# Kernel tuning notes

Hardware: AMD Instinct MI355X
Metric: run time of the kernel (lower is better)

## Reference

```python
import jax, jax.numpy as jnp
import numpy as np

N = 100000      # nodes
E = 1600000     # edges
F_IN = 128
HID = 64
N_CLS = 40


def setup_inputs() -> dict:
    key = jax.random.key(0)
    ks = jax.random.split(key, 8)
    x = jax.random.normal(ks[0], (N, F_IN), dtype=jnp.float32)
    edge_index = jax.random.randint(ks[1], (2, E), 0, N, dtype=jnp.int64)
    # SAGEConv params: lin_l (applied to mean-aggregated neighbors, with bias),
    # lin_r (applied to root/self features, no bias). Glorot-ish init scaling.
    W1_l = jax.random.normal(ks[2], (F_IN, HID), dtype=jnp.float32) / np.sqrt(F_IN)
    b1 = jnp.zeros((HID,), dtype=jnp.float32)
    W1_r = jax.random.normal(ks[3], (F_IN, HID), dtype=jnp.float32) / np.sqrt(F_IN)
    W2_l = jax.random.normal(ks[4], (HID, N_CLS), dtype=jnp.float32) / np.sqrt(HID)
    b2 = jnp.zeros((N_CLS,), dtype=jnp.float32)
    W2_r = jax.random.normal(ks[5], (HID, N_CLS), dtype=jnp.float32) / np.sqrt(HID)
    return {"x": x, "edge_index": edge_index,
            "W1_l": W1_l, "b1": b1, "W1_r": W1_r,
            "W2_l": W2_l, "b2": b2, "W2_r": W2_r}


def _sage_conv(x, src, dst, W_l, b_l, W_r):
    # mean aggregation of neighbor features: messages flow src -> dst
    msgs = x[src]                                              # [E, d]
    summed = jax.ops.segment_sum(msgs, dst, num_segments=N)    # [N, d]
    cnt = jax.ops.segment_sum(jnp.ones((src.shape[0],), x.dtype), dst,
                              num_segments=N)                  # [N]
    agg = summed / jnp.maximum(cnt, 1.0)[:, None]
    return agg @ W_l + b_l + x @ W_r


def reference(x, edge_index, W1_l, b1, W1_r, W2_l, b2, W2_r):
    src, dst = edge_index[0], edge_index[1]
    h = jax.nn.relu(_sage_conv(x, src, dst, W1_l, b1, W1_r))
    # dropout: identity in eval mode
    logits = _sage_conv(h, src, dst, W2_l, b2, W2_r)
    return jax.nn.log_softmax(logits, axis=1)
```

## Files before the change

### kernel.cpp

```cpp
#include <hip/hip_runtime.h>
#include <math.h>

#define N_NODES 100000
#define F_IN    128
#define HID     64
#define N_CLS   40
#define MT      (N_NODES / 16)

#define BSHIFT  9
#define BSZ     512
#define NB      ((N_NODES + BSZ - 1) / BSZ)
#define EPB     4096

typedef __attribute__((ext_vector_type(8))) short bf8_t;
typedef __attribute__((ext_vector_type(4))) float f4_t;
typedef __attribute__((ext_vector_type(2))) float f2v_t;

typedef unsigned short ushort_t;
typedef unsigned int uint_t;
typedef unsigned char uchar_t;

__device__ __forceinline__ ushort_t f2b(float f) {
    union { float f; uint_t u; } c; c.f = f;
    uint_t u = c.u + 0x7FFFu + ((c.u >> 16) & 1u);
    return (ushort_t)(u >> 16);
}
__device__ __forceinline__ float b2f(ushort_t h) {
    union { uint_t u; float f; } c; c.u = ((uint_t)h) << 16;
    return c.f;
}

#if defined(__has_builtin)
#if __has_builtin(__builtin_amdgcn_cvt_pk_f32_fp8) && __has_builtin(__builtin_amdgcn_cvt_pk_fp8_f32)
#define HAVE_FP8_HW 1
#endif
#endif

__device__ __forceinline__ uchar_t fp8_enc(float v) {
#ifdef HAVE_FP8_HW
    return (uchar_t)(__builtin_amdgcn_cvt_pk_fp8_f32(v, v, 0, false) & 0xff);
#else
    union { float f; uint_t u; } c; c.f = v;
    uint_t s = c.u >> 31;
    float av = fabsf(v);
    if (av > 448.f) av = 448.f;
    int e;
    float m = frexpf(av, &e);
    int ee = e + 6;
    uchar_t r;
    if (av == 0.f) r = 0;
    else if (ee <= 0) {
        int q = (int)(av * 512.f + 0.5f);
        if (q > 7) q = 7;
        r = (uchar_t)q;
    } else {
        int q = (int)(m * 16.f + 0.5f);
        if (q == 16) { q = 8; ee += 1; }
        if (ee > 15) { ee = 15; q = 15; }
        r = (uchar_t)((ee << 3) | (q & 7));
    }
    return r | (uchar_t)(s << 7);
#endif
}

__device__ __forceinline__ f2v_t fp8x2_dec_lo(uint_t w) {
#ifdef HAVE_FP8_HW
    return __builtin_amdgcn_cvt_pk_f32_fp8(w, false);
#else
    f2v_t r;
    for (int k = 0; k < 2; ++k) {
        uchar_t b = (w >> (8 * k)) & 0xff;
        uint_t s = (b >> 7) & 1, e = (b >> 3) & 15, m = b & 7;
        float f;
        if (e) { union { uint_t u; float ff; } c;
                 c.u = (s << 31) | ((e + 120) << 23) | (m << 20); f = c.ff; }
        else   { f = (float)m * 0.001953125f; if (s) f = -f; }
        r[k] = f;
    }
    return r;
#endif
}
__device__ __forceinline__ f2v_t fp8x2_dec_hi(uint_t w) {
#ifdef HAVE_FP8_HW
    return __builtin_amdgcn_cvt_pk_f32_fp8(w, true);
#else
    return fp8x2_dec_lo(w >> 16);
#endif
}

__global__ void block_hist_kernel(const int* __restrict__ ei, int E,
                                  int* __restrict__ blockHist) {
    __shared__ int cnt[NB];
    int t = threadIdx.x, blk = blockIdx.x;
    for (int i = t; i < NB; i += 256) cnt[i] = 0;
    __syncthreads();
    int e0 = blk * EPB;
#pragma unroll
    for (int i = 0; i < EPB / 256; ++i) {
        int e = e0 + i * 256 + t;
        if (e < E) atomicAdd(&cnt[ei[E + e] >> BSHIFT], 1);
    }
    __syncthreads();
    for (int i = t; i < NB; i += 256) blockHist[blk * NB + i] = cnt[i];
}

__global__ void col_scan_kernel(const int* __restrict__ blockHist, int nblk,
                                int* __restrict__ blockBase,
                                int* __restrict__ btot) {
    __shared__ int ss[256];
    __shared__ int carry;
    int bin = blockIdx.x, t = threadIdx.x;
    if (t == 0) carry = 0;
    __syncthreads();
    for (int c0 = 0; c0 < nblk; c0 += 256) {
        int b = c0 + t;
        int v = (b < nblk) ? blockHist[b * NB + bin] : 0;
        ss[t] = v;
        __syncthreads();
        for (int off = 1; off < 256; off <<= 1) {
            int u = (t >= off) ? ss[t - off] : 0;
            __syncthreads();
            ss[t] += u;
            __syncthreads();
        }
        if (b < nblk) blockBase[b * NB + bin] = carry + ss[t] - v;
        __syncthreads();
        if (t == 255) carry += ss[255];
        __syncthreads();
    }
    if (t == 0) btot[bin] = carry;
}

__global__ void bucket_scan_kernel(const int* __restrict__ btot,
                                   int* __restrict__ boff,
                                   int* __restrict__ rowptr) {
    __shared__ int ss[256];
    int t = threadIdx.x;
    int v = (t < NB) ? btot[t] : 0;
    ss[t] = v;
    __syncthreads();
    for (int off = 1; off < 256; off <<= 1) {
        int u = (t >= off) ? ss[t - off] : 0;
        __syncthreads();
        ss[t] += u;
        __syncthreads();
    }
    if (t < NB) boff[t] = ss[t] - v;
    if (t == NB - 1) rowptr[N_NODES] = ss[t];
}

__global__ void scatter_pairs_kernel(const int* __restrict__ ei, int E,
                                     const int* __restrict__ blockBase,
                                     const int* __restrict__ boff,
                                     uint_t* __restrict__ pairs) {
    __shared__ int cur[NB];
    __shared__ int base[NB];
    int t = threadIdx.x, blk = blockIdx.x;
    for (int i = t; i < NB; i += 256) {
        cur[i] = 0;
        base[i] = boff[i] + blockBase[blk * NB + i];
    }
    __syncthreads();
    int e0 = blk * EPB;
#pragma unroll
    for (int i = 0; i < EPB / 256; ++i) {
        int e = e0 + i * 256 + t;
        if (e < E) {
            int src = ei[e];
            int dst = ei[E + e];
            int bin = dst >> BSHIFT;
            int r = atomicAdd(&cur[bin], 1);
            pairs[base[bin] + r] = ((uint_t)src << BSHIFT) | (uint_t)(dst & (BSZ - 1));
        }
    }
}

__global__ void bucket_sort_kernel(const uint_t* __restrict__ pairs,
                                   const int* __restrict__ boff,
                                   const int* __restrict__ btot,
                                   int* __restrict__ rowptr,
                                   int* __restrict__ csr) {
    __shared__ int hist[BSZ];
    __shared__ int lofs[BSZ];
    int bin = blockIdx.x, t = threadIdx.x;
    int base = boff[bin], cnt = btot[bin];
    hist[t] = 0;
    __syncthreads();
    for (int i = t; i < cnt; i += BSZ)
        atomicAdd(&hist[pairs[base + i] & (BSZ - 1)], 1);
    __syncthreads();
    int v = hist[t];
    lofs[t] = v;
    __syncthreads();
    for (int off = 1; off < BSZ; off <<= 1) {
        int u = (t >= off) ? lofs[t - off] : 0;
        __syncthreads();
        lofs[t] += u;
        __syncthreads();
    }
    int excl = lofs[t] - v;
    int d_global = (bin << BSHIFT) + t;
    if (d_global < N_NODES) rowptr[d_global] = base + excl;
    __syncthreads();
    lofs[t] = excl;
    hist[t] = 0;
    __syncthreads();
    for (int i = t; i < cnt; i += BSZ) {
        uint_t p = pairs[base + i];
        int lb = p & (BSZ - 1);
        int r = atomicAdd(&hist[lb], 1);
        csr[base + lofs[lb] + r] = (int)(p >> BSHIFT);
    }
}

__global__ void cvt_w_kernel(const float* __restrict__ W1l,
                             const float* __restrict__ W1r,
                             const float* __restrict__ W2l,
                             const float* __restrict__ W2r,
                             ushort_t* __restrict__ W1t,
                             ushort_t* __restrict__ W2t) {
    int t = blockIdx.x * blockDim.x + threadIdx.x;
    if (t < 128 * F_IN) {
        int n = t / F_IN, k = t - n * F_IN;
        float v = (n < HID) ? W1l[k * HID + n] : W1r[k * HID + (n - HID)];
        W1t[t] = f2b(v);
    } else if (t < 128 * F_IN + 80 * HID) {
        int u = t - 128 * F_IN;
        int n = u / HID, k = u - n * HID;
        float v = (n < N_CLS) ? W2l[k * N_CLS + n] : W2r[k * N_CLS + (n - N_CLS)];
        W2t[u] = f2b(v);
    }
}

__global__ void gemm1_mfma_kernel(const float* __restrict__ x,
                                  const ushort_t* __restrict__ W1t,
                                  uchar_t* __restrict__ y1a,
                                  uchar_t* __restrict__ y1b,
                                  ushort_t* __restrict__ z1b) {
    int gid = blockIdx.x * blockDim.x + threadIdx.x;
    int wave = gid >> 6, lane = gid & 63;
    if (wave >= MT) return;
    int m0 = wave * 16;
    int r = lane & 15, q = lane >> 4;

    const float* xr = x + (size_t)(m0 + r) * F_IN + q * 8;
    bf8_t a[4];
#pragma unroll
    for (int kt = 0; kt < 4; ++kt) {
        float4 u = *(const float4*)(xr + kt * 32);
        float4 v = *(const float4*)(xr + kt * 32 + 4);
        bf8_t t;
        t[0] = (short)f2b(u.x); t[1] = (short)f2b(u.y);
        t[2] = (short)f2b(u.z); t[3] = (short)f2b(u.w);
        t[4] = (short)f2b(v.x); t[5] = (short)f2b(v.y);
        t[6] = (short)f2b(v.z); t[7] = (short)f2b(v.w);
        a[kt] = t;
    }
#pragma unroll
    for (int tn = 0; tn < 8; ++tn) {
        const ushort_t* wr = W1t + (size_t)(tn * 16 + r) * F_IN + q * 8;
        f4_t acc = {0.f, 0.f, 0.f, 0.f};
#pragma unroll
        for (int kt = 0; kt < 4; ++kt) {
            bf8_t b = *(const bf8_t*)(wr + kt * 32);
            acc = __builtin_amdgcn_mfma_f32_16x16x32_bf16(a[kt], b, acc, 0, 0, 0);
        }
        int col = tn * 16 + r;
        if (col < 32) {
#pragma unroll
            for (int rr = 0; rr < 4; ++rr) {
                int row = m0 + q * 4 + rr;
                y1a[(size_t)row * 32 + col] = fp8_enc(acc[rr]);
            }
        } else if (col < HID) {
#pragma unroll
            for (int rr = 0; rr < 4; ++rr) {
                int row = m0 + q * 4 + rr;
                y1b[(size_t)row * 32 + (col - 32)] = fp8_enc(acc[rr]);
            }
        } else {
#pragma unroll
            for (int rr = 0; rr < 4; ++rr) {
                int row = m0 + q * 4 + rr;
                z1b[(size_t)row * HID + (col - HID)] = f2b(acc[rr]);
            }
        }
    }
}

__global__ void agg1_half_kernel(const int* __restrict__ rowptr,
                                 const int* __restrict__ csr,
                                 const uchar_t* __restrict__ y1h,
                                 const ushort_t* __restrict__ z1b,
                                 const float* __restrict__ b1,
                                 ushort_t* __restrict__ hb, int half) {
    int gid = blockIdx.x * blockDim.x + threadIdx.x;
    int wave = gid >> 6, lane = gid & 63;
    int g = lane >> 3, l = lane & 7;
    int n = wave * 8 + g;
    if (n >= N_NODES) return;
    int beg = rowptr[n], end = rowptr[n + 1];
    float a0 = 0.f, a1 = 0.f, a2 = 0.f, a3 = 0.f;
    int i = beg;
    for (; i + 3 < end; i += 4) {
        int s0 = csr[i], s1 = csr[i + 1], s2 = csr[i + 2], s3 = csr[i + 3];
        uint_t w0 = *(const uint_t*)(y1h + (size_t)s0 * 32 + l * 4);
        uint_t w1 = *(const uint_t*)(y1h + (size_t)s1 * 32 + l * 4);
        uint_t w2 = *(const uint_t*)(y1h + (size_t)s2 * 32 + l * 4);
        uint_t w3 = *(const uint_t*)(y1h + (size_t)s3 * 32 + l * 4);
        f2v_t p0 = fp8x2_dec_lo(w0), p1 = fp8x2_dec_hi(w0);
        f2v_t q0 = fp8x2_dec_lo(w1), q1 = fp8x2_dec_hi(w1);
        f2v_t r0 = fp8x2_dec_lo(w2), r1 = fp8x2_dec_hi(w2);
        f2v_t t0 = fp8x2_dec_lo(w3), t1 = fp8x2_dec_hi(w3);
        a0 += (p0[0] + q0[0]) + (r0[0] + t0[0]);
        a1 += (p0[1] + q0[1]) + (r0[1] + t0[1]);
        a2 += (p1[0] + q1[0]) + (r1[0] + t1[0]);
        a3 += (p1[1] + q1[1]) + (r1[1] + t1[1]);
    }
    for (; i < end; ++i) {
        uint_t w = *(const uint_t*)(y1h + (size_t)csr[i] * 32 + l * 4);
        f2v_t p0 = fp8x2_dec_lo(w), p1 = fp8x2_dec_hi(w);
        a0 += p0[0]; a1 += p0[1]; a2 += p1[0]; a3 += p1[1];
    }
    float inv = 1.0f / fmaxf((float)(end - beg), 1.0f);
    int c = half * 32 + l * 4;
    float4 bb = *(const float4*)(b1 + c);
    ushort4 zz = *(const ushort4*)(z1b + (size_t)n * HID + c);
    float r0 = fmaxf(fmaf(a0, inv, bb.x + b2f(zz.x)), 0.f);
    float r1 = fmaxf(fmaf(a1, inv, bb.y + b2f(zz.y)), 0.f);
    float r2 = fmaxf(fmaf(a2, inv, bb.z + b2f(zz.z)), 0.f);
    float r3 = fmaxf(fmaf(a3, inv, bb.w + b2f(zz.w)), 0.f);
    ushort4 o;
    o.x = f2b(r0); o.y = f2b(r1); o.z = f2b(r2); o.w = f2b(r3);
    *(ushort4*)(hb + (size_t)n * HID + c) = o;
}

__global__ void gemm2_mfma_kernel(const ushort_t* __restrict__ hb,
                                  const ushort_t* __restrict__ W2t,
                                  uchar_t* __restrict__ y2f8,
                                  ushort_t* __restrict__ z2b) {
    int gid = blockIdx.x * blockDim.x + threadIdx.x;
    int wave = gid >> 6, lane = gid & 63;
    if (wave >= MT) return;
    int m0 = wave * 16;
    int r = lane & 15, q = lane >> 4;

    const ushort_t* hr = hb + (size_t)(m0 + r) * HID + q * 8;
    bf8_t a[2];
#pragma unroll
    for (int kt = 0; kt < 2; ++kt)
        a[kt] = *(const bf8_t*)(hr + kt * 32);

#pragma unroll
    for (int tn = 0; tn < 5; ++tn) {
        const ushort_t* wr = W2t + (size_t)(tn * 16 + r) * HID + q * 8;
        f4_t acc = {0.f, 0.f, 0.f, 0.f};
#pragma unroll
        for (int kt = 0; kt < 2; ++kt) {
            bf8_t b = *(const bf8_t*)(wr + kt * 32);
            acc = __builtin_amdgcn_mfma_f32_16x16x32_bf16(a[kt], b, acc, 0, 0, 0);
        }
        int col = tn * 16 + r;
        if (col < N_CLS) {
#pragma unroll
            for (int rr = 0; rr < 4; ++rr) {
                int row = m0 + q * 4 + rr;
                y2f8[(size_t)row * 40 + col] = fp8_enc(acc[rr]);
            }
        } else {
#pragma unroll
            for (int rr = 0; rr < 4; ++rr) {
                int row = m0 + q * 4 + rr;
                z2b[(size_t)row * HID + (col - N_CLS)] = f2b(acc[rr]);
            }
        }
    }
}

__global__ void agg2_kernel(const int* __restrict__ rowptr,
                            const int* __restrict__ csr,
                            const uchar_t* __restrict__ y2f8,
                            const ushort_t* __restrict__ z2b,
                            const float* __restrict__ b2,
                            float* __restrict__ out) {
    int gid = blockIdx.x * blockDim.x + threadIdx.x;
    int wave = gid >> 6, lane = gid & 63;
    int g = lane >> 4, l = lane & 15;
    int n = wave * 4 + g;
    if (n >= N_NODES) return;
    int beg = rowptr[n], end = rowptr[n + 1];
    float a0 = 0.f, a1 = 0.f, a2 = 0.f, a3 = 0.f;
    int i = beg;
    for (; i + 3 < end; i += 4) {
        int s0 = csr[i], s1 = csr[i + 1], s2 = csr[i + 2], s3 = csr[i + 3];
        uint_t w0 = *(const uint_t*)(y2f8 + (size_t)s0 * 40 + l * 4);
        uint_t w1 = *(const uint_t*)(y2f8 + (size_t)s1 * 40 + l * 4);
        uint_t w2 = *(const uint_t*)(y2f8 + (size_t)s2 * 40 + l * 4);
        uint_t w3 = *(const uint_t*)(y2f8 + (size_t)s3 * 40 + l * 4);
        f2v_t p0 = fp8x2_dec_lo(w0), p1 = fp8x2_dec_hi(w0);
        f2v_t q0 = fp8x2_dec_lo(w1), q1 = fp8x2_dec_hi(w1);
        f2v_t r0 = fp8x2_dec_lo(w2), r1 = fp8x2_dec_hi(w2);
        f2v_t t0 = fp8x2_dec_lo(w3), t1 = fp8x2_dec_hi(w3);
        a0 += (p0[0] + q0[0]) + (r0[0] + t0[0]);
        a1 += (p0[1] + q0[1]) + (r0[1] + t0[1]);
        a2 += (p1[0] + q1[0]) + (r1[0] + t1[0]);
        a3 += (p1[1] + q1[1]) + (r1[1] + t1[1]);
    }
    for (; i < end; ++i) {
        uint_t w = *(const uint_t*)(y2f8 + (size_t)csr[i] * 40 + l * 4);
        f2v_t p0 = fp8x2_dec_lo(w), p1 = fp8x2_dec_hi(w);
        a0 += p0[0]; a1 += p0[1]; a2 += p1[0]; a3 += p1[1];
    }
    float inv = 1.0f / fmaxf((float)(end - beg), 1.0f);
    int c0 = l * 4;
    float4 bb = (l < 10) ? *(const float4*)(b2 + c0)
                         : make_float4(0.f, 0.f, 0.f, 0.f);
    ushort4 zz = *(const ushort4*)(z2b + (size_t)n * HID + c0);
    float v0 = (c0 + 0 < N_CLS) ? fmaf(a0, inv, bb.x + b2f(zz.x)) : -INFINITY;
    float v1 = (c0 + 1 < N_CLS) ? fmaf(a1, inv, bb.y + b2f(zz.y)) : -INFINITY;
    float v2 = (c0 + 2 < N_CLS) ? fmaf(a2, inv, bb.z + b2f(zz.z)) : -INFINITY;
    float v3 = (c0 + 3 < N_CLS) ? fmaf(a3, inv, bb.w + b2f(zz.w)) : -INFINITY;

    float m = fmaxf(fmaxf(v0, v1), fmaxf(v2, v3));
#pragma unroll
    for (int off = 1; off < 16; off <<= 1)
        m = fmaxf(m, __shfl_xor(m, off, 64));
    float s = 0.f;
    if (v0 > -INFINITY) s += expf(v0 - m);
    if (v1 > -INFINITY) s += expf(v1 - m);
    if (v2 > -INFINITY) s += expf(v2 - m);
    if (v3 > -INFINITY) s += expf(v3 - m);
#pragma unroll
    for (int off = 1; off < 16; off <<= 1)
        s += __shfl_xor(s, off, 64);
    float ls = logf(s);
    if (l < 10) {
        float4 o = make_float4(v0 - m - ls, v1 - m - ls, v2 - m - ls, v3 - m - ls);
        *(float4*)(out + (size_t)n * N_CLS + c0) = o;
    }
}

extern "C" void kernel_launch(void* const* d_in, const int* in_sizes, int n_in,
                              void* d_out, int out_size, void* d_ws, size_t ws_size,
                              hipStream_t stream) {
    const float* x   = (const float*)d_in[0];
    const int*   ei  = (const int*)d_in[1];
    const float* W1l = (const float*)d_in[2];
    const float* b1  = (const float*)d_in[3];
    const float* W1r = (const float*)d_in[4];
    const float* W2l = (const float*)d_in[5];
    const float* b2  = (const float*)d_in[6];
    const float* W2r = (const float*)d_in[7];
    float* out = (float*)d_out;
    const int E = in_sizes[1] / 2;
    const int nblk = (E + EPB - 1) / EPB;

    char* p = (char*)d_ws;
    auto take = [&](size_t bytes) {
        char* q = p;
        p += (bytes + 15) & ~(size_t)15;
        return (void*)q;
    };
    int* rowptr     = (int*)take(sizeof(int) * (N_NODES + 4));
    int* blockHist  = (int*)take(sizeof(int) * (size_t)nblk * NB);
    int* blockBase  = (int*)take(sizeof(int) * (size_t)nblk * NB);
    int* btot       = (int*)take(sizeof(int) * NB);
    int* boff       = (int*)take(sizeof(int) * NB);
    uint_t* pairs   = (uint_t*)take(sizeof(uint_t) * (size_t)E);
    int* csr        = (int*)take(sizeof(int) * (size_t)E);
    ushort_t* W1t   = (ushort_t*)take(sizeof(ushort_t) * 128 * F_IN);
    ushort_t* W2t   = (ushort_t*)take(sizeof(ushort_t) * 80 * HID);
    uchar_t* y1a    = (uchar_t*)take(sizeof(uchar_t) * (size_t)N_NODES * 32);
    uchar_t* y1b    = (uchar_t*)take(sizeof(uchar_t) * (size_t)N_NODES * 32);
    ushort_t* z1b   = (ushort_t*)take(sizeof(ushort_t) * (size_t)N_NODES * HID);
    ushort_t* hb    = (ushort_t*)take(sizeof(ushort_t) * (size_t)N_NODES * HID);
    uchar_t* y2f8 = y1a;
    ushort_t* z2b = z1b;

    const int B = 256;

    block_hist_kernel<<<nblk, 256, 0, stream>>>(ei, E, blockHist);
    col_scan_kernel<<<NB, 256, 0, stream>>>(blockHist, nblk, blockBase, btot);
    bucket_scan_kernel<<<1, 256, 0, stream>>>(btot, boff, rowptr);
    scatter_pairs_kernel<<<nblk, 256, 0, stream>>>(ei, E, blockBase, boff, pairs);
    bucket_sort_kernel<<<NB, BSZ, 0, stream>>>(pairs, boff, btot, rowptr, csr);

    cvt_w_kernel<<<(128 * F_IN + 80 * HID + B - 1) / B, B, 0, stream>>>(
        W1l, W1r, W2l, W2r, W1t, W2t);

    int t_mfma = MT * 64;
    int t_agg1 = (N_NODES / 8) * 64;
    int t_agg2 = (N_NODES / 4) * 64;

    gemm1_mfma_kernel<<<(t_mfma + B - 1) / B, B, 0, stream>>>(x, W1t, y1a, y1b, z1b);
    agg1_half_kernel<<<(t_agg1 + B - 1) / B, B, 0, stream>>>(rowptr, csr, y1a, z1b, b1, hb, 0);
    agg1_half_kernel<<<(t_agg1 + B - 1) / B, B, 0, stream>>>(rowptr, csr, y1b, z1b, b1, hb, 1);
    gemm2_mfma_kernel<<<(t_mfma + B - 1) / B, B, 0, stream>>>(hb, W2t, y2f8, z2b);
    agg2_kernel<<<(t_agg2 + B - 1) / B, B, 0, stream>>>(rowptr, csr, y2f8, z2b, b2, out);
}
```

Before: 266.9 us.

## Stage GEMM outputs in LDS for coalesced stores, fold bucket scan into consumers

Measured after the change: 259.6 us. 2.8% less time.

```diff
diff --git a/kernel.cpp b/kernel.cpp
--- a/kernel.cpp
+++ b/kernel.cpp
@@ -131,34 +131,26 @@
     if (t == 0) btot[bin] = carry;
 }
 
-__global__ void bucket_scan_kernel(const int* __restrict__ btot,
-                                   int* __restrict__ boff,
-                                   int* __restrict__ rowptr) {
-    __shared__ int ss[256];
-    int t = threadIdx.x;
-    int v = (t < NB) ? btot[t] : 0;
-    ss[t] = v;
-    __syncthreads();
-    for (int off = 1; off < 256; off <<= 1) {
-        int u = (t >= off) ? ss[t - off] : 0;
-        __syncthreads();
-        ss[t] += u;
-        __syncthreads();
-    }
-    if (t < NB) boff[t] = ss[t] - v;
-    if (t == NB - 1) rowptr[N_NODES] = ss[t];
-}
-
 __global__ void scatter_pairs_kernel(const int* __restrict__ ei, int E,
                                      const int* __restrict__ blockBase,
-                                     const int* __restrict__ boff,
+                                     const int* __restrict__ btot,
                                      uint_t* __restrict__ pairs) {
     __shared__ int cur[NB];
     __shared__ int base[NB];
+    __shared__ int ss[256];
     int t = threadIdx.x, blk = blockIdx.x;
-    for (int i = t; i < NB; i += 256) {
-        cur[i] = 0;
-        base[i] = boff[i] + blockBase[blk * NB + i];
+    int v = (t < NB) ? btot[t] : 0;
+    ss[t] = v;
+    __syncthreads();
+    for (int off = 1; off < 256; off <<= 1) {
+        int u = (t >= off) ? ss[t - off] : 0;
+        __syncthreads();
+        ss[t] += u;
+        __syncthreads();
+    }
+    if (t < NB) {
+        cur[t] = 0;
+        base[t] = (ss[t] - v) + blockBase[blk * NB + t];
     }
     __syncthreads();
     int e0 = blk * EPB;
@@ -176,14 +168,24 @@
 }
 
 __global__ void bucket_sort_kernel(const uint_t* __restrict__ pairs,
-                                   const int* __restrict__ boff,
                                    const int* __restrict__ btot,
                                    int* __restrict__ rowptr,
                                    int* __restrict__ csr) {
     __shared__ int hist[BSZ];
     __shared__ int lofs[BSZ];
     int bin = blockIdx.x, t = threadIdx.x;
-    int base = boff[bin], cnt = btot[bin];
+    int pv = (t < NB) ? btot[t] : 0;
+    lofs[t] = pv;
+    __syncthreads();
+    for (int off = 1; off < BSZ; off <<= 1) {
+        int u = (t >= off) ? lofs[t - off] : 0;
+        __syncthreads();
+        lofs[t] += u;
+        __syncthreads();
+    }
+    int base = (bin > 0) ? lofs[bin - 1] : 0;
+    int cnt = btot[bin];
+    __syncthreads();
     hist[t] = 0;
     __syncthreads();
     for (int i = t; i < cnt; i += BSZ)
@@ -201,6 +203,7 @@
     int excl = lofs[t] - v;
     int d_global = (bin << BSHIFT) + t;
     if (d_global < N_NODES) rowptr[d_global] = base + excl;
+    if (bin == NB - 1 && t == 0) rowptr[N_NODES] = base + cnt;
     __syncthreads();
     lofs[t] = excl;
     hist[t] = 0;
@@ -237,54 +240,60 @@
                                   uchar_t* __restrict__ y1a,
                                   uchar_t* __restrict__ y1b,
                                   ushort_t* __restrict__ z1b) {
-    int gid = blockIdx.x * blockDim.x + threadIdx.x;
-    int wave = gid >> 6, lane = gid & 63;
-    if (wave >= MT) return;
-    int m0 = wave * 16;
-    int r = lane & 15, q = lane >> 4;
-
-    const float* xr = x + (size_t)(m0 + r) * F_IN + q * 8;
-    bf8_t a[4];
-#pragma unroll
-    for (int kt = 0; kt < 4; ++kt) {
-        float4 u = *(const float4*)(xr + kt * 32);
-        float4 v = *(const float4*)(xr + kt * 32 + 4);
-        bf8_t t;
-        t[0] = (short)f2b(u.x); t[1] = (short)f2b(u.y);
-        t[2] = (short)f2b(u.z); t[3] = (short)f2b(u.w);
-        t[4] = (short)f2b(v.x); t[5] = (short)f2b(v.y);
-        t[6] = (short)f2b(v.z); t[7] = (short)f2b(v.w);
-        a[kt] = t;
-    }
-#pragma unroll
-    for (int tn = 0; tn < 8; ++tn) {
-        const ushort_t* wr = W1t + (size_t)(tn * 16 + r) * F_IN + q * 8;
-        f4_t acc = {0.f, 0.f, 0.f, 0.f};
+    __shared__ uchar_t sy[64][80];
+    __shared__ ushort_t sz[64][72];
+    int tid = threadIdx.x;
+    int wave = tid >> 6, lane = tid & 63;
+    int tile = blockIdx.x * 4 + wave;
+    int m0b = blockIdx.x * 64;
+    if (tile < MT) {
+        int m0 = tile * 16;
+        int r = lane & 15, q = lane >> 4;
+        const float* xr = x + (size_t)(m0 + r) * F_IN + q * 8;
+        bf8_t a[4];
 #pragma unroll
         for (int kt = 0; kt < 4; ++kt) {
-            bf8_t b = *(const bf8_t*)(wr + kt * 32);
-            acc = __builtin_amdgcn_mfma_f32_16x16x32_bf16(a[kt], b, acc, 0, 0, 0);
-        }
-        int col = tn * 16 + r;
-        if (col < 32) {
-#pragma unroll
-            for (int rr = 0; rr < 4; ++rr) {
-                int row = m0 + q * 4 + rr;
-                y1a[(size_t)row * 32 + col] = fp8_enc(acc[rr]);
+            float4 u = *(const float4*)(xr + kt * 32);
+            float4 v = *(const float4*)(xr + kt * 32 + 4);
+            bf8_t tt;
+            tt[0] = (short)f2b(u.x); tt[1] = (short)f2b(u.y);
+            tt[2] = (short)f2b(u.z); tt[3] = (short)f2b(u.w);
+            tt[4] = (short)f2b(v.x); tt[5] = (short)f2b(v.y);
+            tt[6] = (short)f2b(v.z); tt[7] = (short)f2b(v.w);
+            a[kt] = tt;
+        }
+        int lr0 = wave * 16 + q * 4;
+#pragma unroll
+        for (int tn = 0; tn < 8; ++tn) {
+            const ushort_t* wr = W1t + (size_t)(tn * 16 + r) * F_IN + q * 8;
+            f4_t acc = {0.f, 0.f, 0.f, 0.f};
+#pragma unroll
+            for (int kt = 0; kt < 4; ++kt) {
+                bf8_t b = *(const bf8_t*)(wr + kt * 32);
+                acc = __builtin_amdgcn_mfma_f32_16x16x32_bf16(a[kt], b, acc, 0, 0, 0);
             }
-        } else if (col < HID) {
-#pragma unroll
-            for (int rr = 0; rr < 4; ++rr) {
-                int row = m0 + q * 4 + rr;
-                y1b[(size_t)row * 32 + (col - 32)] = fp8_enc(acc[rr]);
+            int col = tn * 16 + r;
+            if (col < 64) {
+#pragma unroll
+                for (int rr = 0; rr < 4; ++rr)
+                    sy[lr0 + rr][col] = fp8_enc(acc[rr]);
+            } else {
+#pragma unroll
+                for (int rr = 0; rr < 4; ++rr)
+                    sz[lr0 + rr][col - 64] = f2b(acc[rr]);
             }
-        } else {
-#pragma unroll
-            for (int rr = 0; rr < 4; ++rr) {
-                int row = m0 + q * 4 + rr;
-                z1b[(size_t)row * HID + (col - HID)] = f2b(acc[rr]);
-            }
-        }
+        }
+    }
+    __syncthreads();
+    int vrows = N_NODES - m0b; if (vrows > 64) vrows = 64;
+    for (int idx = tid; idx < vrows * 2; idx += 256) {
+        int row = idx >> 1, c = (idx & 1) << 4;
+        *(uint4*)(y1a + (size_t)(m0b + row) * 32 + c) = *(const uint4*)&sy[row][c];
+        *(uint4*)(y1b + (size_t)(m0b + row) * 32 + c) = *(const uint4*)&sy[row][c + 32];
+    }
+    for (int idx = tid; idx < vrows * 8; idx += 256) {
+        int row = idx >> 3, c = (idx & 7) << 3;
+        *(uint4*)(z1b + (size_t)(m0b + row) * HID + c) = *(const uint4*)&sz[row][c];
     }
 }
 
@@ -339,41 +348,50 @@
                                   const ushort_t* __restrict__ W2t,
                                   uchar_t* __restrict__ y2f8,
                                   ushort_t* __restrict__ z2b) {
-    int gid = blockIdx.x * blockDim.x + threadIdx.x;
-    int wave = gid >> 6, lane = gid & 63;
-    if (wave >= MT) return;
-    int m0 = wave * 16;
-    int r = lane & 15, q = lane >> 4;
-
-    const ushort_t* hr = hb + (size_t)(m0 + r) * HID + q * 8;
-    bf8_t a[2];
-#pragma unroll
-    for (int kt = 0; kt < 2; ++kt)
-        a[kt] = *(const bf8_t*)(hr + kt * 32);
-
-#pragma unroll
-    for (int tn = 0; tn < 5; ++tn) {
-        const ushort_t* wr = W2t + (size_t)(tn * 16 + r) * HID + q * 8;
-        f4_t acc = {0.f, 0.f, 0.f, 0.f};
-#pragma unroll
-        for (int kt = 0; kt < 2; ++kt) {
-            bf8_t b = *(const bf8_t*)(wr + kt * 32);
-            acc = __builtin_amdgcn_mfma_f32_16x16x32_bf16(a[kt], b, acc, 0, 0, 0);
-        }
-        int col = tn * 16 + r;
-        if (col < N_CLS) {
-#pragma unroll
-            for (int rr = 0; rr < 4; ++rr) {
-                int row = m0 + q * 4 + rr;
-                y2f8[(size_t)row * 40 + col] = fp8_enc(acc[rr]);
+    __shared__ uchar_t sy2[64 * 40];
+    __shared__ ushort_t sz2[64][56];
+    int tid = threadIdx.x;
+    int wave = tid >> 6, lane = tid & 63;
+    int tile = blockIdx.x * 4 + wave;
+    int m0b = blockIdx.x * 64;
+    if (tile < MT) {
+        int m0 = tile * 16;
+        int r = lane & 15, q = lane >> 4;
+        const ushort_t* hr = hb + (size_t)(m0 + r) * HID + q * 8;
+        bf8_t a[2];
+#pragma unroll
+        for (int kt = 0; kt < 2; ++kt)
+            a[kt] = *(const bf8_t*)(hr + kt * 32);
+        int lr0 = wave * 16 + q * 4;
+#pragma unroll
+        for (int tn = 0; tn < 5; ++tn) {
+            const ushort_t* wr = W2t + (size_t)(tn * 16 + r) * HID + q * 8;
+            f4_t acc = {0.f, 0.f, 0.f, 0.f};
+#pragma unroll
+            for (int kt = 0; kt < 2; ++kt) {
+                bf8_t b = *(const bf8_t*)(wr + kt * 32);
+                acc = __builtin_amdgcn_mfma_f32_16x16x32_bf16(a[kt], b, acc, 0, 0, 0);
             }
-        } else {
-#pragma unroll
-            for (int rr = 0; rr < 4; ++rr) {
-                int row = m0 + q * 4 + rr;
-                z2b[(size_t)row * HID + (col - N_CLS)] = f2b(acc[rr]);
+            int col = tn * 16 + r;
+            if (col < N_CLS) {
+#pragma unroll
+                for (int rr = 0; rr < 4; ++rr)
+                    sy2[(lr0 + rr) * 40 + col] = fp8_enc(acc[rr]);
+            } else {
+#pragma unroll
+                for (int rr = 0; rr < 4; ++rr)
+                    sz2[lr0 + rr][col - N_CLS] = f2b(acc[rr]);
             }
         }
+    }
+    __syncthreads();
+    int vrows = N_NODES - m0b; if (vrows > 64) vrows = 64;
+    int nch = (vrows * 40) >> 4;
+    for (int idx = tid; idx < nch; idx += 256)
+        *(uint4*)(y2f8 + (size_t)m0b * 40 + idx * 16) = *(const uint4*)&sy2[idx * 16];
+    for (int idx = tid; idx < vrows * 5; idx += 256) {
+        int row = idx / 5, c = (idx - row * 5) * 8;
+        *(uint4*)(z2b + (size_t)(m0b + row) * HID + c) = *(const uint4*)&sz2[row][c];
     }
 }
 
@@ -390,32 +408,35 @@
     if (n >= N_NODES) return;
     int beg = rowptr[n], end = rowptr[n + 1];
     float a0 = 0.f, a1 = 0.f, a2 = 0.f, a3 = 0.f;
-    int i = beg;
-    for (; i + 3 < end; i += 4) {
-        int s0 = csr[i], s1 = csr[i + 1], s2 = csr[i + 2], s3 = csr[i + 3];
-        uint_t w0 = *(const uint_t*)(y2f8 + (size_t)s0 * 40 + l * 4);
-        uint_t w1 = *(const uint_t*)(y2f8 + (size_t)s1 * 40 + l * 4);
-        uint_t w2 = *(const uint_t*)(y2f8 + (size_t)s2 * 40 + l * 4);
-        uint_t w3 = *(const uint_t*)(y2f8 + (size_t)s3 * 40 + l * 4);
-        f2v_t p0 = fp8x2_dec_lo(w0), p1 = fp8x2_dec_hi(w0);
-        f2v_t q0 = fp8x2_dec_lo(w1), q1 = fp8x2_dec_hi(w1);
-        f2v_t r0 = fp8x2_dec_lo(w2), r1 = fp8x2_dec_hi(w2);
-        f2v_t t0 = fp8x2_dec_lo(w3), t1 = fp8x2_dec_hi(w3);
-        a0 += (p0[0] + q0[0]) + (r0[0] + t0[0]);
-        a1 += (p0[1] + q0[1]) + (r0[1] + t0[1]);
-        a2 += (p1[0] + q1[0]) + (r1[0] + t1[0]);
-        a3 += (p1[1] + q1[1]) + (r1[1] + t1[1]);
-    }
-    for (; i < end; ++i) {
-        uint_t w = *(const uint_t*)(y2f8 + (size_t)csr[i] * 40 + l * 4);
-        f2v_t p0 = fp8x2_dec_lo(w), p1 = fp8x2_dec_hi(w);
-        a0 += p0[0]; a1 += p0[1]; a2 += p1[0]; a3 += p1[1];
+    float4 bb = make_float4(0.f, 0.f, 0.f, 0.f);
+    ushort4 zz; zz.x = 0; zz.y = 0; zz.z = 0; zz.w = 0;
+    int c0 = l * 4;
+    if (l < 10) {
+        int i = beg;
+        for (; i + 3 < end; i += 4) {
+            int s0 = csr[i], s1 = csr[i + 1], s2 = csr[i + 2], s3 = csr[i + 3];
+            uint_t w0 = *(const uint_t*)(y2f8 + (size_t)s0 * 40 + c0);
+            uint_t w1 = *(const uint_t*)(y2f8 + (size_t)s1 * 40 + c0);
+            uint_t w2 = *(const uint_t*)(y2f8 + (size_t)s2 * 40 + c0);
+            uint_t w3 = *(const uint_t*)(y2f8 + (size_t)s3 * 40 + c0);
+            f2v_t p0 = fp8x2_dec_lo(w0), p1 = fp8x2_dec_hi(w0);
+            f2v_t q0 = fp8x2_dec_lo(w1), q1 = fp8x2_dec_hi(w1);
+            f2v_t r0 = fp8x2_dec_lo(w2), r1 = fp8x2_dec_hi(w2);
+            f2v_t t0 = fp8x2_dec_lo(w3), t1 = fp8x2_dec_hi(w3);
+            a0 += (p0[0] + q0[0]) + (r0[0] + t0[0]);
+            a1 += (p0[1] + q0[1]) + (r0[1] + t0[1]);
+            a2 += (p1[0] + q1[0]) + (r1[0] + t1[0]);
+            a3 += (p1[1] + q1[1]) + (r1[1] + t1[1]);
+        }
+        for (; i < end; ++i) {
+            uint_t w = *(const uint_t*)(y2f8 + (size_t)csr[i] * 40 + c0);
+            f2v_t p0 = fp8x2_dec_lo(w), p1 = fp8x2_dec_hi(w);
+            a0 += p0[0]; a1 += p0[1]; a2 += p1[0]; a3 += p1[1];
+        }
+        bb = *(const float4*)(b2 + c0);
+        zz = *(const ushort4*)(z2b + (size_t)n * HID + c0);
     }
     float inv = 1.0f / fmaxf((float)(end - beg), 1.0f);
-    int c0 = l * 4;
-    float4 bb = (l < 10) ? *(const float4*)(b2 + c0)
-                         : make_float4(0.f, 0.f, 0.f, 0.f);
-    ushort4 zz = *(const ushort4*)(z2b + (size_t)n * HID + c0);
     float v0 = (c0 + 0 < N_CLS) ? fmaf(a0, inv, bb.x + b2f(zz.x)) : -INFINITY;
     float v1 = (c0 + 1 < N_CLS) ? fmaf(a1, inv, bb.y + b2f(zz.y)) : -INFINITY;
     float v2 = (c0 + 2 < N_CLS) ? fmaf(a2, inv, bb.z + b2f(zz.z)) : -INFINITY;
@@ -465,7 +486,6 @@
     int* blockHist  = (int*)take(sizeof(int) * (size_t)nblk * NB);
     int* blockBase  = (int*)take(sizeof(int) * (size_t)nblk * NB);
     int* btot       = (int*)take(sizeof(int) * NB);
-    int* boff       = (int*)take(sizeof(int) * NB);
     uint_t* pairs   = (uint_t*)take(sizeof(uint_t) * (size_t)E);
     int* csr        = (int*)take(sizeof(int) * (size_t)E);
     ushort_t* W1t   = (ushort_t*)take(sizeof(ushort_t) * 128 * F_IN);
@@ -481,20 +501,19 @@
 
     block_hist_kernel<<<nblk, 256, 0, stream>>>(ei, E, blockHist);
     col_scan_kernel<<<NB, 256, 0, stream>>>(blockHist, nblk, blockBase, btot);
-    bucket_scan_kernel<<<1, 256, 0, stream>>>(btot, boff, rowptr);
-    scatter_pairs_kernel<<<nblk, 256, 0, stream>>>(ei, E, blockBase, boff, pairs);
-    bucket_sort_kernel<<<NB, BSZ, 0, stream>>>(pairs, boff, btot, rowptr, csr);
+    scatter_pairs_kernel<<<nblk, 256, 0, stream>>>(ei, E, blockBase, btot, pairs);
+    bucket_sort_kernel<<<NB, BSZ, 0, stream>>>(pairs, btot, rowptr, csr);
 
     cvt_w_kernel<<<(128 * F_IN + 80 * HID + B - 1) / B, B, 0, stream>>>(
         W1l, W1r, W2l, W2r, W1t, W2t);
 
-    int t_mfma = MT * 64;
+    int gemm_blocks = (MT + 3) / 4;
     int t_agg1 = (N_NODES / 8) * 64;
     int t_agg2 = (N_NODES / 4) * 64;
 
-    gemm1_mfma_kernel<<<(t_mfma + B - 1) / B, B, 0, stream>>>(x, W1t, y1a, y1b, z1b);
+    gemm1_mfma_kernel<<<gemm_blocks, B, 0, stream>>>(x, W1t, y1a, y1b, z1b);
     agg1_half_kernel<<<(t_agg1 + B - 1) / B, B, 0, stream>>>(rowptr, csr, y1a, z1b, b1, hb, 0);
     agg1_half_kernel<<<(t_agg1 + B - 1) / B, B, 0, stream>>>(rowptr, csr, y1b, z1b, b1, hb, 1);
-    gemm2_mfma_kernel<<<(t_mfma + B - 1) / B, B, 0, stream>>>(hb, W2t, y2f8, z2b);
+    gemm2_mfma_kernel<<<gemm_blocks, B, 0, stream>>>(hb, W2t, y2f8, z2b);
     agg2_kernel<<<(t_agg2 + B - 1) / B, B, 0, stream>>>(rowptr, csr, y2f8, z2b, b2, out);
 }
```
